# Performance work log

Hardware: AMD Instinct MI355X
Metric: run time of the kernel (lower is better)

The kernel has to match this reference:

```python
import jax, jax.numpy as jnp
import numpy as np
from jax.scipy.special import i0

B, P = 2, 524288
N = (512, 512)            # uniform frequency grid
M = 4                     # window cutoff m (2M taps per dim)
SIGMA = 2.0
NGRID = tuple(2 * (int(SIGMA * Ni) // 2) for Ni in N)  # oversampled grid (1024, 1024)
BETA = tuple(float(np.pi * (2.0 - 1.0 / (ng / Ni))) for ng, Ni in zip(NGRID, N))


def _phi_hat_1d(Ni, ni, b):
    # Fourier coefficients of the Kaiser-Bessel window, k = -Ni/2 .. Ni/2-1
    k = jnp.arange(-Ni // 2, Ni // 2, dtype=jnp.float32)
    arg = jnp.sqrt(b * b - (2.0 * jnp.pi * k / ni) ** 2)
    return i0(M * arg) / ni


def _window_ft():
    # separable d-dim Fourier coefficient grid, shape [N1, N2] (== window.ft)
    c1 = _phi_hat_1d(N[0], NGRID[0], BETA[0])
    c2 = _phi_hat_1d(N[1], NGRID[1], BETA[1])
    return c1[:, None] * c2[None, :]


def _phi(t, ni, b):
    # Kaiser-Bessel window in time domain, support |t| <= M/ni
    u2 = M * M - (ni * t) ** 2
    u = jnp.sqrt(jnp.maximum(u2, 1e-12))
    return jnp.where(u2 > 0, jnp.sinh(b * u) / (jnp.pi * u), 0.0)


def setup_inputs() -> dict:
    key = jax.random.key(0)
    k1, k2 = jax.random.split(key)
    x = jax.random.uniform(k1, (B, P, 2), jnp.float32, -0.5, 0.5)  # points on torus
    f_hat = jax.random.normal(k2, (B, N[0], N[1], 2), jnp.float32)  # complex as [re,im]
    return {"x": x, "f_hat": f_hat}


def _nfft_forward(x, f_hat):
    # f(x_j) ~= sum_k f_hat[k] exp(-2 pi i <k, x_j>) via window-deconvolved oversampled FFT + local gather
    fh = (f_hat[..., 0] + 1j * f_hat[..., 1]).astype(jnp.complex64)  # [B, N1, N2]
    ft = _window_ft().astype(jnp.float32)
    gh = fh / ft                                                    # deconvolve
    p1 = (NGRID[0] - N[0]) // 2
    p2 = (NGRID[1] - N[1]) // 2
    gh = jnp.pad(gh, ((0, 0), (p1, p1), (p2, p2)))                  # centered zero-pad to n
    g = jnp.fft.fftn(jnp.fft.ifftshift(gh, axes=(-2, -1)), axes=(-2, -1))
    g = g / (NGRID[0] * NGRID[1])                                   # g_l = (1/n) sum_k gh_k e^{-2pi i kl/n}

    offs = jnp.arange(-M + 1, M + 1)                                # [2M]
    ws, idxs = [], []
    for d in range(2):
        nd = NGRID[d]
        xd = x[..., d]                                              # [B, P]
        l0 = jnp.floor(xd * nd).astype(jnp.int32)
        l = l0[..., None] + offs                                    # [B, P, 2M]
        t = xd[..., None] - l.astype(jnp.float32) / nd
        ws.append(_phi(t, nd, BETA[d]))
        idxs.append(jnp.mod(l, nd))

    g_flat = g.reshape(B, NGRID[0] * NGRID[1])
    acc = jnp.zeros((B, P), jnp.complex64)
    for i in range(2 * M):                                          # fixed 2m x 2m taps
        for j in range(2 * M):
            flat = idxs[0][..., i] * NGRID[1] + idxs[1][..., j]     # [B, P]
            gv = jnp.take_along_axis(g_flat, flat, axis=1)
            acc = acc + (ws[0][..., i] * ws[1][..., j]) * gv
    return jnp.stack([acc.real, acc.imag], axis=-1)                 # [B, P, 2]


def reference(x, f_hat):
    return _nfft_forward(x, f_hat)
```

## Files before the change

kernel.cpp:

```cpp
#include <hip/hip_runtime.h>

constexpr int   NGRID = 1024;
constexpr int   BATCH = 2;
constexpr int   NPTS  = 524288;
constexpr int   BINS  = 2048;
constexpr int   CAP   = 768;
constexpr float BETA  = 4.71238898038469f;
constexpr float PI_F  = 3.14159265358979f;

#define PIDX(i) ((i) + ((i) >> 4))

constexpr size_t G_BYTES  = (size_t)BATCH * NGRID * NGRID * sizeof(float2);
constexpr size_t GCNT_OFF = G_BYTES;
constexpr size_t PERM_OFF = G_BYTES + 8192;

__device__ __forceinline__ float i0f_large(float x) {
    float t = 3.75f / x;
    float p =  0.00392377f;
    p = p * t + -0.01647633f;
    p = p * t +  0.02635537f;
    p = p * t + -0.02057706f;
    p = p * t +  0.00916281f;
    p = p * t + -0.00157565f;
    p = p * t +  0.00225319f;
    p = p * t +  0.01328592f;
    p = p * t +  0.39894228f;
    return __expf(x) * rsqrtf(x) * p;
}

__device__ __forceinline__ int tile_of(float2 xv, int b) {
    int c1 = ((int)floorf(xv.x * 1024.0f)) & 1023;
    int c2 = ((int)floorf(xv.y * 1024.0f)) & 1023;
    return (b << 10) + ((c1 >> 5) << 5) + (c2 >> 5);
}

__global__ __launch_bounds__(1024) void bin_kernel(const float2* __restrict__ x,
                                                   int* __restrict__ gcnt,
                                                   int* __restrict__ perm) {
    __shared__ int h[BINS];
    int tid = threadIdx.x;
    h[tid] = 0; h[tid + 1024] = 0;
    __syncthreads();

    int base = blockIdx.x * 8192;
    int tile[8];
    #pragma unroll
    for (int i = 0; i < 8; ++i) {
        int gid = base + tid + i * 1024;
        tile[i] = tile_of(x[gid], gid >> 19);
        atomicAdd(&h[tile[i]], 1);
    }
    __syncthreads();

    int c0 = h[tid], c1 = h[tid + 1024];
    int b0 = c0 ? atomicAdd(&gcnt[tid], c0) : 0;
    int b1 = c1 ? atomicAdd(&gcnt[tid + 1024], c1) : 0;
    __syncthreads();
    h[tid] = b0; h[tid + 1024] = b1;
    __syncthreads();

    #pragma unroll
    for (int i = 0; i < 8; ++i) {
        int pos = atomicAdd(&h[tile[i]], 1);
        perm[tile[i] * CAP + pos] = base + tid + i * 1024;
    }
}

__device__ __forceinline__ void build_tw(float2* T, int tid, int nthreads) {
    for (int idx = tid; idx < 1024; idx += nthreads) {
        if (idx == 0) { T[0] = make_float2(1.f, 0.f); continue; }
        int k = 31 - __clz(idx);
        int j = idx - (1 << k);
        float ang = (-PI_F) * (float)j / (float)(1 << k);
        float sw, cw;
        __sincosf(ang, &sw, &cw);
        T[idx] = make_float2(cw, sw);
    }
}

__device__ __forceinline__ void fft1024(float2* s, const float2* T) {
    int tid = threadIdx.x;
    for (int k = 9; k >= 0; --k) {
        int half = 1 << k;
        __syncthreads();
        #pragma unroll
        for (int r = 0; r < 2; ++r) {
            int t    = tid + (r << 8);
            int j    = t & (half - 1);
            int base = ((t >> k) << (k + 1)) + j;
            int pb = PIDX(base), ph = PIDX(base + half);
            float2 a = s[pb];
            float2 c = s[ph];
            float2 d = make_float2(a.x - c.x, a.y - c.y);
            float2 w = T[half + j];
            s[pb] = make_float2(a.x + c.x, a.y + c.y);
            s[ph] = make_float2(d.x * w.x - d.y * w.y,
                                d.x * w.y + d.y * w.x);
        }
    }
    __syncthreads();
}

__global__ __launch_bounds__(256) void fft_rows(const float2* __restrict__ fh,
                                                float2* __restrict__ g) {
    __shared__ float2 s[1087];
    __shared__ float2 T[1024];
    int blk = blockIdx.x;
    int row = (blk < 256) ? blk : blk + 512;
    int b = blockIdx.y;
    int a1 = (row + 256) & 1023;
    int tid = threadIdx.x;

    build_tw(T, tid, 256);

    float k1 = (float)(a1 - 256);
    float w1 = (2.0f * PI_F / 1024.0f) * k1;
    float c1 = i0f_large(4.0f * sqrtf(BETA * BETA - w1 * w1));

    const float2* fr = fh + ((long)b << 18) + ((long)a1 << 9);

    float w2a = (2.0f * PI_F / 1024.0f) * (float)tid;
    float c2a = i0f_large(4.0f * sqrtf(BETA * BETA - w2a * w2a));
    float w2b = (2.0f * PI_F / 1024.0f) * (float)(tid - 256);
    float c2b = i0f_large(4.0f * sqrtf(BETA * BETA - w2b * w2b));

    float2 va = fr[tid + 256];
    float2 vb = fr[tid];
    float ia = 1.0f / (c1 * c2a);
    float ib = 1.0f / (c1 * c2b);
    s[PIDX(tid)]       = make_float2(va.x * ia, va.y * ia);
    s[PIDX(tid + 256)] = make_float2(0.f, 0.f);
    s[PIDX(tid + 512)] = make_float2(0.f, 0.f);
    s[PIDX(tid + 768)] = make_float2(vb.x * ib, vb.y * ib);

    fft1024(s, T);

    float2* base = g + ((long)b << 20) + ((long)row << 10);
    #pragma unroll
    for (int i = 0; i < 4; ++i) {
        int idx = tid + (i << 8);
        unsigned rev = __brev((unsigned)idx) >> 22;
        base[idx] = s[PIDX(rev)];
    }
}

__global__ __launch_bounds__(256) void fft_cols(float2* __restrict__ g) {
    constexpr int STR = 1092;
    __shared__ float2 s[4 * STR];
    __shared__ float2 T[1024];
    int b  = blockIdx.y;
    int C0 = blockIdx.x * 4;
    int t  = threadIdx.x;
    int c  = t & 3, L = t >> 2;
    float2* gb = g + ((long)b << 20);

    build_tw(T, t, 256);

    float2* sf = s + c * STR;
    #pragma unroll
    for (int i = 0; i < 4; ++i) {
        int r = L + i * 64;
        sf[PIDX(r)] = gb[((long)r << 10) + C0 + c];
    }
    #pragma unroll
    for (int i = 0; i < 4; ++i) {
        int r = L + i * 64 + 768;
        sf[PIDX(r)] = gb[((long)r << 10) + C0 + c];
    }
    #pragma unroll
    for (int i = 0; i < 8; ++i) {
        int r = L + i * 64 + 256;
        sf[PIDX(r)] = make_float2(0.f, 0.f);
    }

    for (int k = 9; k >= 0; --k) {
        int half = 1 << k;
        __syncthreads();
        #pragma unroll
        for (int rr = 0; rr < 8; ++rr) {
            int bt   = L + rr * 64;
            int j    = bt & (half - 1);
            int base = ((bt >> k) << (k + 1)) + j;
            int pb = PIDX(base), ph = PIDX(base + half);
            float2 a  = sf[pb];
            float2 cc = sf[ph];
            float2 d  = make_float2(a.x - cc.x, a.y - cc.y);
            float2 w  = T[half + j];
            sf[pb] = make_float2(a.x + cc.x, a.y + cc.y);
            sf[ph] = make_float2(d.x * w.x - d.y * w.y,
                                 d.x * w.y + d.y * w.x);
        }
    }
    __syncthreads();

    #pragma unroll
    for (int i = 0; i < 16; ++i) {
        int r = L + i * 64;
        unsigned rev = __brev((unsigned)r) >> 22;
        gb[((long)r << 10) + C0 + c] = sf[PIDX(rev)];
    }
}

__global__ __launch_bounds__(256) void gather_binned(const float2* __restrict__ x,
                                                     const float2* __restrict__ g,
                                                     const int* __restrict__ gcnt,
                                                     const int* __restrict__ perm,
                                                     float2* __restrict__ out) {
    __shared__ float2 patch[37 * 37];
    int tb = blockIdx.x;
    int b  = tb >> 10;
    int tt = tb & 1023;
    int tR = tt >> 5, tC = tt & 31;
    int R0 = (tR << 5) - 2, C0 = (tC << 5) - 2;
    const float2* gb = g + ((long)b << 20);

    for (int p = threadIdx.x; p < 37 * 37; p += 256) {
        int pr = p / 37, pc = p - pr * 37;
        int gr = (R0 + pr) & 1023, gc = (C0 + pc) & 1023;
        patch[p] = gb[(gr << 10) + gc];
    }
    __syncthreads();

    int cnt = gcnt[tb];
    if (cnt > CAP) cnt = CAP;
    int off0 = tb * CAP;
    for (int i = (int)threadIdx.x; i < cnt; i += 256) {
        int gid = perm[off0 + i];
        float2 xv = x[gid];

        float w1[6], w2[6];
        int rr0, cc0;
        {
            float xs = xv.x * 1024.0f;
            float fl = floorf(xs);
            float fr = xs - fl;
            rr0 = (((int)fl) & 1023) - (tR << 5);
            #pragma unroll
            for (int k = 0; k < 6; ++k) {
                float tv = fr - (float)(k - 2);
                float u2 = 16.0f - tv * tv;
                float ir = rsqrtf(u2);
                float z  = BETA * u2 * ir;
                float E  = __expf(z);
                float sh = E - __builtin_amdgcn_rcpf(E);
                w1[k] = sh * 0.159154943f * ir;
            }
        }
        {
            float xs = xv.y * 1024.0f;
            float fl = floorf(xs);
            float fr = xs - fl;
            cc0 = (((int)fl) & 1023) - (tC << 5);
            #pragma unroll
            for (int k = 0; k < 6; ++k) {
                float tv = fr - (float)(k - 2);
                float u2 = 16.0f - tv * tv;
                float ir = rsqrtf(u2);
                float z  = BETA * u2 * ir;
                float E  = __expf(z);
                float sh = E - __builtin_amdgcn_rcpf(E);
                w2[k] = sh * 0.159154943f * ir;
            }
        }

        float ar = 0.0f, ai = 0.0f;
        #pragma unroll
        for (int ii = 0; ii < 6; ++ii) {
            int pbase = (rr0 + ii) * 37 + cc0;
            float wi = w1[ii];
            #pragma unroll
            for (int jj = 0; jj < 6; ++jj) {
                float2 gv = patch[pbase + jj];
                float w = wi * w2[jj];
                ar = fmaf(w, gv.x, ar);
                ai = fmaf(w, gv.y, ai);
            }
        }
        out[gid] = make_float2(ar, ai);
    }
}

extern "C" void kernel_launch(void* const* d_in, const int* in_sizes, int n_in,
                              void* d_out, int out_size, void* d_ws, size_t ws_size,
                              hipStream_t stream) {
    const float2* x  = (const float2*)d_in[0];
    const float2* fh = (const float2*)d_in[1];
    char* ws = (char*)d_ws;
    float2* g   = (float2*)ws;
    int* gcnt   = (int*)(ws + GCNT_OFF);
    int* perm   = (int*)(ws + PERM_OFF);

    hipMemsetAsync(gcnt, 0, BINS * sizeof(int), stream);
    bin_kernel<<<dim3((BATCH * NPTS) / 8192), dim3(1024), 0, stream>>>(x, gcnt, perm);

    fft_rows<<<dim3(512, BATCH), dim3(256), 0, stream>>>(fh, g);
    fft_cols<<<dim3(256, BATCH), dim3(256), 0, stream>>>(g);

    gather_binned<<<dim3(BINS), dim3(256), 0, stream>>>(x, g, gcnt, perm, (float2*)d_out);
}
```

Before: 131.8 us.

## Switch shared-memory FFTs to radix-4 and drop negligible exp(-z) in sinh

Row and column 1024-point FFTs move from ten radix-2 stages to five radix-4 stages, with a new twiddle table and a base-4 digit-reversal output permutation. This halves the barriers and shared-memory passes per FFT. Separately, the gather window drops the exp(-z) term of sinh, since z is at least about 12 there and the term is negligible. That trades a tiny accuracy change for fewer reciprocal operations per tap.

```diff
diff --git a/kernel.cpp b/kernel.cpp
--- a/kernel.cpp
+++ b/kernel.cpp
@@ -34,6 +34,15 @@
     return (b << 10) + ((c1 >> 5) << 5) + (c2 >> 5);
 }
 
+__device__ __forceinline__ float2 cmul(float2 a, float2 w) {
+    return make_float2(a.x * w.x - a.y * w.y, a.x * w.y + a.y * w.x);
+}
+
+__device__ __forceinline__ int digitrev4_10(int f) {
+    unsigned r = __brev((unsigned)f) >> 22;
+    return (int)(((r & 0x2AAu) >> 1) | ((r & 0x155u) << 1));
+}
+
 __global__ __launch_bounds__(1024) void bin_kernel(const float2* __restrict__ x,
                                                    int* __restrict__ gcnt,
                                                    int* __restrict__ perm) {
@@ -66,52 +75,55 @@
     }
 }
 
-__device__ __forceinline__ void build_tw(float2* T, int tid, int nthreads) {
-    for (int idx = tid; idx < 1024; idx += nthreads) {
-        if (idx == 0) { T[0] = make_float2(1.f, 0.f); continue; }
-        int k = 31 - __clz(idx);
-        int j = idx - (1 << k);
-        float ang = (-PI_F) * (float)j / (float)(1 << k);
-        float sw, cw;
-        __sincosf(ang, &sw, &cw);
-        T[idx] = make_float2(cw, sw);
-    }
-}
-
-__device__ __forceinline__ void fft1024(float2* s, const float2* T) {
-    int tid = threadIdx.x;
-    for (int k = 9; k >= 0; --k) {
-        int half = 1 << k;
-        __syncthreads();
-        #pragma unroll
-        for (int r = 0; r < 2; ++r) {
-            int t    = tid + (r << 8);
-            int j    = t & (half - 1);
-            int base = ((t >> k) << (k + 1)) + j;
-            int pb = PIDX(base), ph = PIDX(base + half);
-            float2 a = s[pb];
-            float2 c = s[ph];
-            float2 d = make_float2(a.x - c.x, a.y - c.y);
-            float2 w = T[half + j];
-            s[pb] = make_float2(a.x + c.x, a.y + c.y);
-            s[ph] = make_float2(d.x * w.x - d.y * w.y,
-                                d.x * w.y + d.y * w.x);
+__device__ __forceinline__ void build_tw4(float2* T, int tid, int nthreads) {
+    int off = 0, q = 256, sig = 1;
+    #pragma unroll
+    for (int st = 0; st < 5; ++st) {
+        for (int m = tid; m < 3 * q; m += nthreads) {
+            int sec = 0, j = m;
+            if (j >= q) { sec++; j -= q; }
+            if (j >= q) { sec++; j -= q; }
+            float ang = (-2.0f * PI_F / 1024.0f) * (float)((sec + 1) * j * sig);
+            float sw, cw;
+            __sincosf(ang, &sw, &cw);
+            T[off + m] = make_float2(cw, sw);
         }
-    }
-    __syncthreads();
+        off += 3 * q; q >>= 2; sig <<= 2;
+    }
+}
+
+__device__ __forceinline__ void bfly4(float2* s, const float2* T,
+                                      int bt, int q, int off) {
+    int j    = bt & (q - 1);
+    int base = ((bt - j) << 2) + j;
+    int p0 = PIDX(base), p1 = PIDX(base + q);
+    int p2 = PIDX(base + 2 * q), p3 = PIDX(base + 3 * q);
+    float2 a0 = s[p0], a1 = s[p1], a2 = s[p2], a3 = s[p3];
+    float2 t0 = make_float2(a0.x + a2.x, a0.y + a2.y);
+    float2 t1 = make_float2(a0.x - a2.x, a0.y - a2.y);
+    float2 t2 = make_float2(a1.x + a3.x, a1.y + a3.y);
+    float2 t3 = make_float2(a1.x - a3.x, a1.y - a3.y);
+    float2 b0 = make_float2(t0.x + t2.x, t0.y + t2.y);
+    float2 b2 = make_float2(t0.x - t2.x, t0.y - t2.y);
+    float2 b1 = make_float2(t1.x + t3.y, t1.y - t3.x);
+    float2 b3 = make_float2(t1.x - t3.y, t1.y + t3.x);
+    s[p0] = b0;
+    s[p1] = cmul(b1, T[off + j]);
+    s[p2] = cmul(b2, T[off + q + j]);
+    s[p3] = cmul(b3, T[off + 2 * q + j]);
 }
 
 __global__ __launch_bounds__(256) void fft_rows(const float2* __restrict__ fh,
                                                 float2* __restrict__ g) {
     __shared__ float2 s[1087];
-    __shared__ float2 T[1024];
+    __shared__ float2 T[1023];
     int blk = blockIdx.x;
     int row = (blk < 256) ? blk : blk + 512;
     int b = blockIdx.y;
     int a1 = (row + 256) & 1023;
     int tid = threadIdx.x;
 
-    build_tw(T, tid, 256);
+    build_tw4(T, tid, 256);
 
     float k1 = (float)(a1 - 256);
     float w1 = (2.0f * PI_F / 1024.0f) * k1;
@@ -133,28 +145,34 @@
     s[PIDX(tid + 512)] = make_float2(0.f, 0.f);
     s[PIDX(tid + 768)] = make_float2(vb.x * ib, vb.y * ib);
 
-    fft1024(s, T);
+    int off = 0, q = 256;
+    #pragma unroll
+    for (int st = 0; st < 5; ++st) {
+        __syncthreads();
+        bfly4(s, T, tid, q, off);
+        off += 3 * q; q >>= 2;
+    }
+    __syncthreads();
 
     float2* base = g + ((long)b << 20) + ((long)row << 10);
     #pragma unroll
     for (int i = 0; i < 4; ++i) {
         int idx = tid + (i << 8);
-        unsigned rev = __brev((unsigned)idx) >> 22;
-        base[idx] = s[PIDX(rev)];
+        base[idx] = s[PIDX(digitrev4_10(idx))];
     }
 }
 
 __global__ __launch_bounds__(256) void fft_cols(float2* __restrict__ g) {
     constexpr int STR = 1092;
     __shared__ float2 s[4 * STR];
-    __shared__ float2 T[1024];
+    __shared__ float2 T[1023];
     int b  = blockIdx.y;
     int C0 = blockIdx.x * 4;
     int t  = threadIdx.x;
     int c  = t & 3, L = t >> 2;
     float2* gb = g + ((long)b << 20);
 
-    build_tw(T, t, 256);
+    build_tw4(T, t, 256);
 
     float2* sf = s + c * STR;
     #pragma unroll
@@ -173,31 +191,21 @@
         sf[PIDX(r)] = make_float2(0.f, 0.f);
     }
 
-    for (int k = 9; k >= 0; --k) {
-        int half = 1 << k;
+    int off = 0, q = 256;
+    #pragma unroll
+    for (int st = 0; st < 5; ++st) {
         __syncthreads();
         #pragma unroll
-        for (int rr = 0; rr < 8; ++rr) {
-            int bt   = L + rr * 64;
-            int j    = bt & (half - 1);
-            int base = ((bt >> k) << (k + 1)) + j;
-            int pb = PIDX(base), ph = PIDX(base + half);
-            float2 a  = sf[pb];
-            float2 cc = sf[ph];
-            float2 d  = make_float2(a.x - cc.x, a.y - cc.y);
-            float2 w  = T[half + j];
-            sf[pb] = make_float2(a.x + cc.x, a.y + cc.y);
-            sf[ph] = make_float2(d.x * w.x - d.y * w.y,
-                                 d.x * w.y + d.y * w.x);
-        }
+        for (int rr = 0; rr < 4; ++rr)
+            bfly4(sf, T, L + rr * 64, q, off);
+        off += 3 * q; q >>= 2;
     }
     __syncthreads();
 
     #pragma unroll
     for (int i = 0; i < 16; ++i) {
         int r = L + i * 64;
-        unsigned rev = __brev((unsigned)r) >> 22;
-        gb[((long)r << 10) + C0 + c] = sf[PIDX(rev)];
+        gb[((long)r << 10) + C0 + c] = sf[PIDX(digitrev4_10(r))];
     }
 }
 
@@ -241,9 +249,7 @@
                 float u2 = 16.0f - tv * tv;
                 float ir = rsqrtf(u2);
                 float z  = BETA * u2 * ir;
-                float E  = __expf(z);
-                float sh = E - __builtin_amdgcn_rcpf(E);
-                w1[k] = sh * 0.159154943f * ir;
+                w1[k] = __expf(z) * 0.159154943f * ir;
             }
         }
         {
@@ -257,9 +263,7 @@
                 float u2 = 16.0f - tv * tv;
                 float ir = rsqrtf(u2);
                 float z  = BETA * u2 * ir;
-                float E  = __expf(z);
-                float sh = E - __builtin_amdgcn_rcpf(E);
-                w2[k] = sh * 0.159154943f * ir;
+                w2[k] = __expf(z) * 0.159154943f * ir;
             }
         }
 
```

Result: faster. 126.6 us (-4.0%).
